# Optimization experiments

Hardware: AMD Instinct MI355X
Metric: run time of the kernel (lower is better)

The kernel has to match this reference:

```python
import jax, jax.numpy as jnp
import numpy as np
import math

B, T, D = 2, 2048, 1024
DC, DM, H = 512, 1536, 16
DE, DG = 4096, 1024
EPS = 1e-5
NEG = -1e30


def _layernorm(x, w, b):
    mu = jnp.mean(x, axis=-1, keepdims=True)
    var = jnp.mean(jnp.square(x - mu), axis=-1, keepdims=True)
    return (x - mu) * jax.lax.rsqrt(var + EPS) * w + b


def setup_inputs() -> dict:
    key = jax.random.key(0)
    ks = jax.random.split(key, 12)
    s = 0.02
    x = jax.random.normal(ks[0], (B, T, D), jnp.float32)
    mask = jnp.tril(jnp.ones((T, T), jnp.int32))[None, None]  # [1,1,T,T] causal
    return {
        "x": x,
        "mask": mask,
        "ln1_w": jnp.ones((D,), jnp.float32),
        "ln1_b": jnp.zeros((D,), jnp.float32),
        "wq": jax.random.normal(ks[1], (D, DC), jnp.float32) * s,
        "bq": jnp.zeros((DC,), jnp.float32),
        "wk": jax.random.normal(ks[2], (D, DC), jnp.float32) * s,
        "bk": jnp.zeros((DC,), jnp.float32),
        "wv": jax.random.normal(ks[3], (D, DM), jnp.float32) * s,
        "bv": jnp.zeros((DM,), jnp.float32),
        "wo": jax.random.normal(ks[4], (DM, D), jnp.float32) * s,
        "bo": jnp.zeros((D,), jnp.float32),
        "ln2_w": jnp.ones((D,), jnp.float32),
        "ln2_b": jnp.zeros((D,), jnp.float32),
        "we": jax.random.normal(ks[5], (D, DE), jnp.float32) * s,
        "be": jnp.zeros((DE,), jnp.float32),
        "wg": jax.random.normal(ks[6], (D, DG), jnp.float32) * s,
        "bg": jnp.zeros((DG,), jnp.float32),
        "wu": jax.random.normal(ks[7], (DG, DE), jnp.float32) * s,
        "bu": jnp.zeros((DE,), jnp.float32),
        "wc": jax.random.normal(ks[8], (DE, D), jnp.float32) * s,
        "bc": jnp.zeros((D,), jnp.float32),
    }


def reference(x, mask, ln1_w, ln1_b, wq, bq, wk, bk, wv, bv, wo, bo,
              ln2_w, ln2_b, we, be, wg, bg, wu, bu, wc, bc):
    b, t, _ = x.shape
    chd, mhd = DC // H, DM // H
    # --- attention sublayer ---
    x1 = _layernorm(x, ln1_w, ln1_b)
    q = (x1 @ wq + bq).reshape(b, t, H, chd).transpose(0, 2, 1, 3)  # [b,h,t,chd]
    k = (x1 @ wk + bk).reshape(b, t, H, chd).transpose(0, 2, 1, 3)
    v = (x1 @ wv + bv).reshape(b, t, H, mhd).transpose(0, 2, 1, 3)  # [b,h,t,mhd]
    sc = jnp.einsum('bhqd,bhkd->bhqk', q, k) / math.sqrt(chd)
    sc = jnp.where(mask == 0, NEG, sc)
    attn = jax.nn.softmax(sc, axis=-1)
    y = jnp.einsum('bhqk,bhkd->bhqd', attn, v)  # [b,h,t,mhd]
    y = y.transpose(0, 2, 1, 3).reshape(b, t, DM)
    x = x + (y @ wo + bo)
    # --- FFN sublayer (double-gated SiLU) ---
    x2 = _layernorm(x, ln2_w, ln2_b)
    e = x2 @ we + be
    g = jax.nn.sigmoid(jax.nn.silu(x2 @ wg + bg) @ wu + bu)
    return x + (jax.nn.silu(e * g) @ wc + bc)
```

## Files before the change

kernel.cpp:

```cpp
#include <hip/hip_runtime.h>
#include <hip/hip_bf16.h>

typedef __bf16 bf16x8_t __attribute__((ext_vector_type(8)));
typedef float f32x4_t __attribute__((ext_vector_type(4)));

#define B_ 2
#define T_ 2048
#define D_ 1024
#define DC_ 512
#define DM_ 1536
#define H_ 16
#define DE_ 4096
#define DG_ 1024
#define ROWS (B_*T_)
#define QS_ 2560
#define EG_ 5120
#define MB (1u<<20)

#define GPTR(p) ((const __attribute__((address_space(1))) unsigned int*)(p))
#define LPTR(p) ((__attribute__((address_space(3))) unsigned int*)(p))

__device__ __forceinline__ float sigmoid_f(float x) { return 1.f / (1.f + __expf(-x)); }

__global__ __launch_bounds__(256)
void transpose_cast(const float* __restrict__ W, __hip_bfloat16* __restrict__ Wt,
                    int K, int N) {
    __shared__ float t[32][33];
    const int n0 = blockIdx.x * 32, k0 = blockIdx.y * 32;
    const int tx = threadIdx.x, ty = threadIdx.y;
#pragma unroll
    for (int r = 0; r < 4; ++r)
        t[ty + r * 8][tx] = W[(size_t)(k0 + ty + r * 8) * N + n0 + tx];
    __syncthreads();
#pragma unroll
    for (int r = 0; r < 4; ++r)
        Wt[(size_t)(n0 + ty + r * 8) * K + k0 + tx] = __float2bfloat16(t[tx][ty + r * 8]);
}

__global__ __launch_bounds__(256)
void concat_bias3(const float* __restrict__ a, int na, const float* __restrict__ b,
                  int nb, const float* __restrict__ c, int n, float* __restrict__ o) {
    const int i = blockIdx.x * 256 + threadIdx.x;
    if (i < n)
        o[i] = i < na ? a[i] : (i < na + nb ? b[i - na] : c[i - na - nb]);
}

__global__ __launch_bounds__(256)
void transpose_v(const __hip_bfloat16* __restrict__ QKV, __hip_bfloat16* __restrict__ Vt) {
    __shared__ __hip_bfloat16 t[32][33];
    const int bh = blockIdx.z;
    const int b = bh >> 4, h = bh & 15;
    const int t0 = blockIdx.x * 32;
    const int d0 = blockIdx.y * 32;
    const int tx = threadIdx.x, ty = threadIdx.y;
#pragma unroll
    for (int r = 0; r < 4; ++r)
        t[ty + r * 8][tx] = QKV[(size_t)(b * T_ + t0 + ty + r * 8) * QS_ + 1024 + h * 96 + d0 + tx];
    __syncthreads();
#pragma unroll
    for (int r = 0; r < 4; ++r)
        Vt[((size_t)bh * 96 + d0 + ty + r * 8) * T_ + t0 + tx] = t[tx][ty + r * 8];
}

__global__ __launch_bounds__(256)
void ln_cast(const float* __restrict__ x, const float* __restrict__ w,
             const float* __restrict__ b, __hip_bfloat16* __restrict__ out) {
    const int row = blockIdx.x;
    const int tid = threadIdx.x;
    const float4 v = ((const float4*)(x + (size_t)row * D_))[tid];
    float s = v.x + v.y + v.z + v.w;
#pragma unroll
    for (int o = 32; o; o >>= 1) s += __shfl_down(s, o);
    __shared__ float red1[4], red2[4];
    if (!(tid & 63)) red1[tid >> 6] = s;
    __syncthreads();
    const float mu = (red1[0] + red1[1] + red1[2] + red1[3]) * (1.f / D_);
    const float dx = v.x - mu, dy = v.y - mu, dz = v.z - mu, dw = v.w - mu;
    float s2 = dx * dx + dy * dy + dz * dz + dw * dw;
#pragma unroll
    for (int o = 32; o; o >>= 1) s2 += __shfl_down(s2, o);
    if (!(tid & 63)) red2[tid >> 6] = s2;
    __syncthreads();
    const float var = (red2[0] + red2[1] + red2[2] + red2[3]) * (1.f / D_);
    const float rs = rsqrtf(var + 1e-5f);
    const float4 wv = ((const float4*)w)[tid];
    const float4 bv = ((const float4*)b)[tid];
    __hip_bfloat16* op = out + (size_t)row * D_ + tid * 4;
    op[0] = __float2bfloat16(dx * rs * wv.x + bv.x);
    op[1] = __float2bfloat16(dy * rs * wv.y + bv.y);
    op[2] = __float2bfloat16(dz * rs * wv.z + bv.z);
    op[3] = __float2bfloat16(dw * rs * wv.w + bv.w);
}

template <int EPI, int BM, int BN>
__global__ __launch_bounds__(256)
void gemm_bt(const __hip_bfloat16* __restrict__ A, const __hip_bfloat16* __restrict__ Bt,
             const float* __restrict__ bias, const float* __restrict__ resid,
             const __hip_bfloat16* __restrict__ Ein,
             void* __restrict__ C0, void* __restrict__ C1, int M, int N, int K) {
    __shared__ __align__(16) __hip_bfloat16 As[BM * 32];
    __shared__ __align__(16) __hip_bfloat16 Bs[BN * 32];
    const int tid = threadIdx.x;
    const int m0 = blockIdx.y * BM;
    const int n0 = blockIdx.x * BN;
    const int lane = tid & 63;
    const int wave = tid >> 6;
    const int wm = (wave >> 1) * (BM / 2), wn = (wave & 1) * (BN / 2);
    const int quad = lane >> 4;
    const int lr = lane & 15;
    constexpr int MI = BM / 32, NJ = BN / 32;

    f32x4_t acc[MI][NJ] = {};

    for (int k0 = 0; k0 < K; k0 += 32) {
#pragma unroll
        for (int p = 0; p < BM / 64; ++p) {
            const int s = p * 256 + tid;
            const int row = s >> 2;
            const int kc2 = (s & 3) ^ ((row >> 1) & 3);
            __builtin_amdgcn_global_load_lds(
                GPTR(A + (size_t)(m0 + row) * K + k0 + kc2 * 8),
                LPTR(&As[s * 8]), 16, 0, 0);
        }
#pragma unroll
        for (int p = 0; p < BN / 64; ++p) {
            const int s = p * 256 + tid;
            const int row = s >> 2;
            const int kc2 = (s & 3) ^ ((row >> 1) & 3);
            __builtin_amdgcn_global_load_lds(
                GPTR(Bt + (size_t)(n0 + row) * K + k0 + kc2 * 8),
                LPTR(&Bs[s * 8]), 16, 0, 0);
        }
        __syncthreads();
        bf16x8_t af[MI], bfr[NJ];
#pragma unroll
        for (int i = 0; i < MI; ++i) {
            const int row = wm + i * 16 + lr;
            af[i] = *(const bf16x8_t*)(&As[(row * 4 + (quad ^ ((row >> 1) & 3))) * 8]);
        }
#pragma unroll
        for (int j = 0; j < NJ; ++j) {
            const int row = wn + j * 16 + lr;
            bfr[j] = *(const bf16x8_t*)(&Bs[(row * 4 + (quad ^ ((row >> 1) & 3))) * 8]);
        }
#pragma unroll
        for (int i = 0; i < MI; ++i)
#pragma unroll
            for (int j = 0; j < NJ; ++j)
                acc[i][j] = __builtin_amdgcn_mfma_f32_16x16x32_bf16(af[i], bfr[j], acc[i][j], 0, 0, 0);
        __syncthreads();
    }

    const int rbase = quad * 4;
#pragma unroll
    for (int j = 0; j < NJ; ++j) {
        const int col = n0 + wn + j * 16 + lr;
        const float bj = bias[col];
#pragma unroll
        for (int i = 0; i < MI; ++i) {
#pragma unroll
            for (int r = 0; r < 4; ++r) {
                const int row = m0 + wm + i * 16 + rbase + r;
                const float v = acc[i][j][r] + bj;
                if (EPI == 0) {
                    ((__hip_bfloat16*)C0)[(size_t)row * N + col] = __float2bfloat16(v);
                } else if (EPI == 1) {
                    const size_t o = (size_t)row * N + col;
                    ((float*)C0)[o] = resid[o] + v;
                } else if (EPI == 4) {
                    const size_t o = (size_t)row * N + col;
                    const float z = __bfloat162float(Ein[o]) * sigmoid_f(v);
                    ((__hip_bfloat16*)C0)[o] = __float2bfloat16(z * sigmoid_f(z));
                } else {
                    if (col < DE_)
                        ((__hip_bfloat16*)C0)[(size_t)row * DE_ + col] = __float2bfloat16(v);
                    else
                        ((__hip_bfloat16*)C1)[(size_t)row * DG_ + (col - DE_)] =
                            __float2bfloat16(v * sigmoid_f(v));
                }
            }
        }
    }
}

__global__ __launch_bounds__(256)
void attn_mfma(const __hip_bfloat16* __restrict__ QKV, const __hip_bfloat16* __restrict__ Vt,
               __hip_bfloat16* __restrict__ Y) {
    __shared__ __hip_bfloat16 Ks[128][40];
    __shared__ __hip_bfloat16 Vts[96][136];
    __shared__ __hip_bfloat16 Ps[4][16][72];
    const int tid = threadIdx.x;
    const int lane = tid & 63;
    const int w = tid >> 6;
    const int c = lane & 15;
    const int quad = lane >> 4;
    const int bh = blockIdx.y;
    const int b = bh >> 4, h = bh & 15;
    const size_t qbase = (size_t)b * T_ * QS_ + h * 32;
    const size_t kbase = qbase + 512;
    const size_t vtbase = (size_t)bh * 96 * T_;
    const size_t ybase = (size_t)b * T_ * DM_ + h * 96;
    const float scale2 = 0.17677669529663687f * 1.4426950408889634f;

    for (int half = 0; half < 2; ++half) {
        const int qt = half ? (31 - (int)blockIdx.x) : (int)blockIdx.x;
        const int q0 = qt * 64;
        const int ntiles = (qt >> 1) + 1;
        const int qrow_a = q0 + w * 16 + c;
        const bf16x8_t qf = *(const bf16x8_t*)(QKV + qbase + (size_t)qrow_a * QS_ + quad * 8);

        f32x4_t o[6] = {};
        float mrow[4], lrow[4];
#pragma unroll
        for (int r = 0; r < 4; ++r) { mrow[r] = -1e30f; lrow[r] = 0.f; }
        const int row_c = q0 + w * 16 + quad * 4;

        for (int t = 0; t < ntiles; ++t) {
            const int k0 = t * 128;
#pragma unroll
            for (int p = 0; p < 2; ++p) {
                const int idx = p * 256 + tid;
                const int kr = idx >> 2, cc = idx & 3;
                *(uint4*)(&Ks[kr][cc * 8]) =
                    *(const uint4*)(QKV + kbase + (size_t)(k0 + kr) * QS_ + cc * 8);
            }
#pragma unroll
            for (int p = 0; p < 6; ++p) {
                const int idx = p * 256 + tid;
                const int vr = idx >> 4, vc = idx & 15;
                *(uint4*)(&Vts[vr][vc * 8]) =
                    *(const uint4*)(Vt + vtbase + (size_t)vr * T_ + k0 + vc * 8);
            }
            __syncthreads();

            f32x4_t s[8];
#pragma unroll
            for (int t2 = 0; t2 < 8; ++t2) {
                const bf16x8_t kf = *(const bf16x8_t*)(&Ks[t2 * 16 + c][quad * 8]);
                f32x4_t z = {0.f, 0.f, 0.f, 0.f};
                s[t2] = __builtin_amdgcn_mfma_f32_16x16x32_bf16(qf, kf, z, 0, 0, 0);
            }

            float p[8][4];
            const bool needmask = (k0 + 128 > q0);
            if (needmask) {
#pragma unroll
                for (int t2 = 0; t2 < 8; ++t2) {
                    const int col = k0 + t2 * 16 + c;
#pragma unroll
                    for (int r = 0; r < 4; ++r) {
                        float v = s[t2][r] * scale2;
                        if (col > row_c + r) v = -1e30f;
                        p[t2][r] = v;
                    }
                }
            } else {
#pragma unroll
                for (int t2 = 0; t2 < 8; ++t2)
#pragma unroll
                    for (int r = 0; r < 4; ++r) p[t2][r] = s[t2][r] * scale2;
            }

#pragma unroll
            for (int r = 0; r < 4; ++r) {
                float mx = p[0][r];
#pragma unroll
                for (int t2 = 1; t2 < 8; ++t2) mx = fmaxf(mx, p[t2][r]);
#pragma unroll
                for (int o2 = 1; o2 < 16; o2 <<= 1) mx = fmaxf(mx, __shfl_xor(mx, o2));
                const float mnew = fmaxf(mrow[r], mx);
                const float alpha = exp2f(mrow[r] - mnew);
                mrow[r] = mnew;
                float rsum = 0.f;
#pragma unroll
                for (int t2 = 0; t2 < 8; ++t2) {
                    p[t2][r] = exp2f(p[t2][r] - mnew);
                    rsum += p[t2][r];
                }
#pragma unroll
                for (int o2 = 1; o2 < 16; o2 <<= 1) rsum += __shfl_xor(rsum, o2);
                lrow[r] = lrow[r] * alpha + rsum;
#pragma unroll
                for (int nb = 0; nb < 6; ++nb) o[nb][r] *= alpha;
            }

#pragma unroll
            for (int hh = 0; hh < 2; ++hh) {
#pragma unroll
                for (int t2 = 0; t2 < 4; ++t2)
#pragma unroll
                    for (int r = 0; r < 4; ++r)
                        Ps[w][quad * 4 + r][t2 * 16 + c] = __float2bfloat16(p[hh * 4 + t2][r]);
                const bf16x8_t pf0 = *(const bf16x8_t*)(&Ps[w][c][quad * 8]);
                const bf16x8_t pf1 = *(const bf16x8_t*)(&Ps[w][c][32 + quad * 8]);
#pragma unroll
                for (int nb = 0; nb < 6; ++nb) {
                    const bf16x8_t vf0 = *(const bf16x8_t*)(&Vts[nb * 16 + c][hh * 64 + quad * 8]);
                    o[nb] = __builtin_amdgcn_mfma_f32_16x16x32_bf16(pf0, vf0, o[nb], 0, 0, 0);
                    const bf16x8_t vf1 = *(const bf16x8_t*)(&Vts[nb * 16 + c][hh * 64 + 32 + quad * 8]);
                    o[nb] = __builtin_amdgcn_mfma_f32_16x16x32_bf16(pf1, vf1, o[nb], 0, 0, 0);
                }
            }
            __syncthreads();
        }

#pragma unroll
        for (int r = 0; r < 4; ++r) {
            const float inv = 1.f / lrow[r];
            const size_t rowoff = ybase + (size_t)(row_c + r) * DM_;
#pragma unroll
            for (int nb = 0; nb < 6; ++nb)
                Y[rowoff + nb * 16 + c] = __float2bfloat16(o[nb][r] * inv);
        }
    }
}

extern "C" void kernel_launch(void* const* d_in, const int* in_sizes, int n_in,
                              void* d_out, int out_size, void* d_ws, size_t ws_size,
                              hipStream_t stream) {
    const float* x     = (const float*)d_in[0];
    const float* ln1_w = (const float*)d_in[2];
    const float* ln1_b = (const float*)d_in[3];
    const float* wq = (const float*)d_in[4];  const float* bq = (const float*)d_in[5];
    const float* wk = (const float*)d_in[6];  const float* bk = (const float*)d_in[7];
    const float* wv = (const float*)d_in[8];  const float* bv = (const float*)d_in[9];
    const float* wo = (const float*)d_in[10]; const float* bo = (const float*)d_in[11];
    const float* ln2_w = (const float*)d_in[12];
    const float* ln2_b = (const float*)d_in[13];
    const float* we = (const float*)d_in[14]; const float* be = (const float*)d_in[15];
    const float* wg = (const float*)d_in[16]; const float* bg = (const float*)d_in[17];
    const float* wu = (const float*)d_in[18]; const float* bu = (const float*)d_in[19];
    const float* wc = (const float*)d_in[20]; const float* bc = (const float*)d_in[21];
    float* out = (float*)d_out;

    char* ws = (char*)d_ws;
    typedef __hip_bfloat16 bf16;
    bf16* wqkvT = (bf16*)(ws + (size_t) 0 * MB);
    bf16* wqT   = wqkvT;
    bf16* wkT   = (bf16*)(ws + (size_t) 1 * MB);
    bf16* wvT   = (bf16*)(ws + (size_t) 2 * MB);
    bf16* woT   = (bf16*)(ws + (size_t) 5 * MB);
    bf16* wewgT = (bf16*)(ws + (size_t) 8 * MB);
    bf16* weT   = wewgT;
    bf16* wgT   = (bf16*)(ws + (size_t)16 * MB);
    bf16* wuT   = (bf16*)(ws + (size_t)18 * MB);
    bf16* wcT   = (bf16*)(ws + (size_t)26 * MB);
    float* bqkv = (float*)(ws + (size_t)34 * MB);
    float* bewg = (float*)(ws + (size_t)34 * MB + 65536);
    bf16* x1b   = (bf16*)(ws + (size_t)35 * MB);
    bf16* x2b   = x1b;
    bf16* qkv   = (bf16*)(ws + (size_t)43 * MB);
    float* xmid = (float*)(ws + (size_t)43 * MB);
    bf16* vt    = (bf16*)(ws + (size_t)63 * MB);
    bf16* yb    = (bf16*)(ws + (size_t)75 * MB);
    bf16* eb    = (bf16*)(ws + (size_t)59 * MB);
    bf16* hb    = (bf16*)(ws + (size_t)91 * MB);

    const dim3 tb(32, 8);
    transpose_cast<<<dim3(DC_ / 32, D_ / 32), tb, 0, stream>>>(wq, wqT, D_, DC_);
    transpose_cast<<<dim3(DC_ / 32, D_ / 32), tb, 0, stream>>>(wk, wkT, D_, DC_);
    transpose_cast<<<dim3(DM_ / 32, D_ / 32), tb, 0, stream>>>(wv, wvT, D_, DM_);
    transpose_cast<<<dim3(D_ / 32, DM_ / 32), tb, 0, stream>>>(wo, woT, DM_, D_);
    transpose_cast<<<dim3(DE_ / 32, D_ / 32), tb, 0, stream>>>(we, weT, D_, DE_);
    transpose_cast<<<dim3(DG_ / 32, D_ / 32), tb, 0, stream>>>(wg, wgT, D_, DG_);
    transpose_cast<<<dim3(DE_ / 32, DG_ / 32), tb, 0, stream>>>(wu, wuT, DG_, DE_);
    transpose_cast<<<dim3(D_ / 32, DE_ / 32), tb, 0, stream>>>(wc, wcT, DE_, D_);
    concat_bias3<<<(QS_ + 255) / 256, 256, 0, stream>>>(bq, 512, bk, 512, bv, QS_, bqkv);
    concat_bias3<<<(EG_ + 255) / 256, 256, 0, stream>>>(be, DE_, bg, DG_, nullptr, EG_, bewg);

    ln_cast<<<ROWS, 256, 0, stream>>>(x, ln1_w, ln1_b, x1b);

    gemm_bt<0, 128, 128><<<dim3(QS_ / 128, ROWS / 128), 256, 0, stream>>>(
        x1b, wqkvT, bqkv, nullptr, nullptr, qkv, nullptr, ROWS, QS_, D_);

    transpose_v<<<dim3(T_ / 32, 3, B_ * H_), tb, 0, stream>>>(qkv, vt);

    attn_mfma<<<dim3(16, B_ * H_), 256, 0, stream>>>(qkv, vt, yb);

    gemm_bt<1, 64, 64><<<dim3(D_ / 64, ROWS / 64), 256, 0, stream>>>(
        yb, woT, bo, x, nullptr, xmid, nullptr, ROWS, D_, DM_);

    ln_cast<<<ROWS, 256, 0, stream>>>(xmid, ln2_w, ln2_b, x2b);

    gemm_bt<5, 128, 128><<<dim3(EG_ / 128, ROWS / 128), 256, 0, stream>>>(
        x2b, wewgT, bewg, nullptr, nullptr, eb, hb, ROWS, EG_, D_);

    gemm_bt<4, 128, 128><<<dim3(DE_ / 128, ROWS / 128), 256, 0, stream>>>(
        hb, wuT, bu, nullptr, eb, eb, nullptr, ROWS, DE_, DG_);

    gemm_bt<1, 64, 64><<<dim3(D_ / 64, ROWS / 64), 256, 0, stream>>>(
        eb, wcT, bc, xmid, nullptr, out, nullptr, ROWS, D_, DE_);
}
```

Measured before the change: 566.5 us.

## Double-buffer GEMM LDS tiles and stage epilogue through LDS for vector stores

The GEMM main loop now uses two LDS buffers, issuing the async global-to-LDS loads for the next K slice before computing the current one, with one barrier per iteration. This hides load latency behind the MFMA work. The epilogue writes accumulators into LDS, then reads them back as 16-byte rows for coalesced vector stores and residual/Ein loads, replacing scattered scalar stores. The cost is more LDS per block, which can reduce occupancy, and the EPI 4 sigmoid result is now rounded to bf16 before the multiply.

```diff
diff --git a/kernel.cpp b/kernel.cpp
--- a/kernel.cpp
+++ b/kernel.cpp
@@ -98,8 +98,17 @@
              const float* __restrict__ bias, const float* __restrict__ resid,
              const __hip_bfloat16* __restrict__ Ein,
              void* __restrict__ C0, void* __restrict__ C1, int M, int N, int K) {
-    __shared__ __align__(16) __hip_bfloat16 As[BM * 32];
-    __shared__ __align__(16) __hip_bfloat16 Bs[BN * 32];
+    constexpr int MI = BM / 32, NJ = BN / 32;
+    constexpr size_t STAGE_BYTES = (size_t)(BM + BN) * 128;
+    constexpr size_t EPI_BYTES = (EPI == 1) ? (size_t)BM * (BN + 4) * 4
+                                            : (size_t)BM * (BN + 8) * 2;
+    constexpr size_t SMEM_BYTES = STAGE_BYTES > EPI_BYTES ? STAGE_BYTES : EPI_BYTES;
+    __shared__ __align__(16) unsigned char smem[SMEM_BYTES];
+    __hip_bfloat16* As0 = (__hip_bfloat16*)smem;
+    __hip_bfloat16* Bs0 = As0 + BM * 32;
+    __hip_bfloat16* As1 = Bs0 + BN * 32;
+    __hip_bfloat16* Bs1 = As1 + BM * 32;
+
     const int tid = threadIdx.x;
     const int m0 = blockIdx.y * BM;
     const int n0 = blockIdx.x * BN;
@@ -108,11 +117,8 @@
     const int wm = (wave >> 1) * (BM / 2), wn = (wave & 1) * (BN / 2);
     const int quad = lane >> 4;
     const int lr = lane & 15;
-    constexpr int MI = BM / 32, NJ = BN / 32;
-
-    f32x4_t acc[MI][NJ] = {};
-
-    for (int k0 = 0; k0 < K; k0 += 32) {
+
+    auto stage = [&](int k0, __hip_bfloat16* Asd, __hip_bfloat16* Bsd) {
 #pragma unroll
         for (int p = 0; p < BM / 64; ++p) {
             const int s = p * 256 + tid;
@@ -120,7 +126,7 @@
             const int kc2 = (s & 3) ^ ((row >> 1) & 3);
             __builtin_amdgcn_global_load_lds(
                 GPTR(A + (size_t)(m0 + row) * K + k0 + kc2 * 8),
-                LPTR(&As[s * 8]), 16, 0, 0);
+                LPTR(Asd + s * 8), 16, 0, 0);
         }
 #pragma unroll
         for (int p = 0; p < BN / 64; ++p) {
@@ -129,55 +135,105 @@
             const int kc2 = (s & 3) ^ ((row >> 1) & 3);
             __builtin_amdgcn_global_load_lds(
                 GPTR(Bt + (size_t)(n0 + row) * K + k0 + kc2 * 8),
-                LPTR(&Bs[s * 8]), 16, 0, 0);
-        }
+                LPTR(Bsd + s * 8), 16, 0, 0);
+        }
+    };
+
+    f32x4_t acc[MI][NJ] = {};
+    stage(0, As0, Bs0);
+    const int kiters = K >> 5;
+    for (int k = 0; k < kiters; ++k) {
         __syncthreads();
+        const __hip_bfloat16* Ar = (k & 1) ? As1 : As0;
+        const __hip_bfloat16* Br = (k & 1) ? Bs1 : Bs0;
+        if (k + 1 < kiters)
+            stage((k + 1) << 5, (k & 1) ? As0 : As1, (k & 1) ? Bs0 : Bs1);
         bf16x8_t af[MI], bfr[NJ];
 #pragma unroll
         for (int i = 0; i < MI; ++i) {
             const int row = wm + i * 16 + lr;
-            af[i] = *(const bf16x8_t*)(&As[(row * 4 + (quad ^ ((row >> 1) & 3))) * 8]);
+            af[i] = *(const bf16x8_t*)(Ar + (row * 4 + (quad ^ ((row >> 1) & 3))) * 8);
         }
 #pragma unroll
         for (int j = 0; j < NJ; ++j) {
             const int row = wn + j * 16 + lr;
-            bfr[j] = *(const bf16x8_t*)(&Bs[(row * 4 + (quad ^ ((row >> 1) & 3))) * 8]);
+            bfr[j] = *(const bf16x8_t*)(Br + (row * 4 + (quad ^ ((row >> 1) & 3))) * 8);
         }
 #pragma unroll
         for (int i = 0; i < MI; ++i)
 #pragma unroll
             for (int j = 0; j < NJ; ++j)
                 acc[i][j] = __builtin_amdgcn_mfma_f32_16x16x32_bf16(af[i], bfr[j], acc[i][j], 0, 0, 0);
+    }
+    __syncthreads();
+
+    if (EPI == 1) {
+        float* Ct = (float*)smem;
+        constexpr int LDC = BN + 4;
+#pragma unroll
+        for (int j = 0; j < NJ; ++j) {
+            const float bj = bias[n0 + wn + j * 16 + lr];
+#pragma unroll
+            for (int i = 0; i < MI; ++i)
+#pragma unroll
+                for (int r = 0; r < 4; ++r)
+                    Ct[(wm + i * 16 + quad * 4 + r) * LDC + wn + j * 16 + lr] =
+                        acc[i][j][r] + bj;
+        }
         __syncthreads();
-    }
-
-    const int rbase = quad * 4;
-#pragma unroll
-    for (int j = 0; j < NJ; ++j) {
-        const int col = n0 + wn + j * 16 + lr;
-        const float bj = bias[col];
-#pragma unroll
-        for (int i = 0; i < MI; ++i) {
-#pragma unroll
-            for (int r = 0; r < 4; ++r) {
-                const int row = m0 + wm + i * 16 + rbase + r;
-                const float v = acc[i][j][r] + bj;
-                if (EPI == 0) {
-                    ((__hip_bfloat16*)C0)[(size_t)row * N + col] = __float2bfloat16(v);
-                } else if (EPI == 1) {
-                    const size_t o = (size_t)row * N + col;
-                    ((float*)C0)[o] = resid[o] + v;
-                } else if (EPI == 4) {
-                    const size_t o = (size_t)row * N + col;
-                    const float z = __bfloat162float(Ein[o]) * sigmoid_f(v);
-                    ((__hip_bfloat16*)C0)[o] = __float2bfloat16(z * sigmoid_f(z));
-                } else {
-                    if (col < DE_)
-                        ((__hip_bfloat16*)C0)[(size_t)row * DE_ + col] = __float2bfloat16(v);
-                    else
-                        ((__hip_bfloat16*)C1)[(size_t)row * DG_ + (col - DE_)] =
-                            __float2bfloat16(v * sigmoid_f(v));
+        constexpr int CH = BN / 4;
+#pragma unroll
+        for (int p = 0; p < BM * CH / 256; ++p) {
+            const int s = p * 256 + tid;
+            const int row = s / CH, ch = s % CH;
+            float4 t = *(const float4*)(&Ct[row * LDC + ch * 4]);
+            const size_t o = (size_t)(m0 + row) * N + n0 + ch * 4;
+            const float4 rv = *(const float4*)(resid + o);
+            t.x += rv.x; t.y += rv.y; t.z += rv.z; t.w += rv.w;
+            *(float4*)((float*)C0 + o) = t;
+        }
+    } else {
+        __hip_bfloat16* Ct = (__hip_bfloat16*)smem;
+        constexpr int LDC = BN + 8;
+        const bool gsilu = (EPI == 5) && (n0 >= DE_);
+#pragma unroll
+        for (int j = 0; j < NJ; ++j) {
+            const float bj = bias[n0 + wn + j * 16 + lr];
+#pragma unroll
+            for (int i = 0; i < MI; ++i)
+#pragma unroll
+                for (int r = 0; r < 4; ++r) {
+                    float v = acc[i][j][r] + bj;
+                    if (EPI == 4) v = sigmoid_f(v);
+                    else if (EPI == 5) { if (gsilu) v = v * sigmoid_f(v); }
+                    Ct[(wm + i * 16 + quad * 4 + r) * LDC + wn + j * 16 + lr] =
+                        __float2bfloat16(v);
                 }
+        }
+        __syncthreads();
+        constexpr int CH = BN / 8;
+#pragma unroll
+        for (int p = 0; p < BM * CH / 256; ++p) {
+            const int s = p * 256 + tid;
+            const int row = s / CH, ch = s % CH;
+            union { uint4 u; __hip_bfloat16 h[8]; } tv, ev, ov;
+            tv.u = *(const uint4*)(&Ct[row * LDC + ch * 8]);
+            if (EPI == 4) {
+                const size_t o = (size_t)(m0 + row) * N + n0 + ch * 8;
+                ev.u = *(const uint4*)(Ein + o);
+#pragma unroll
+                for (int q = 0; q < 8; ++q) {
+                    const float z = __bfloat162float(ev.h[q]) * __bfloat162float(tv.h[q]);
+                    ov.h[q] = __float2bfloat16(z * sigmoid_f(z));
+                }
+                *(uint4*)((__hip_bfloat16*)C0 + o) = ov.u;
+            } else if (EPI == 5) {
+                if (n0 < DE_)
+                    *(uint4*)((__hip_bfloat16*)C0 + (size_t)(m0 + row) * DE_ + n0 + ch * 8) = tv.u;
+                else
+                    *(uint4*)((__hip_bfloat16*)C1 + (size_t)(m0 + row) * DG_ + (n0 - DE_) + ch * 8) = tv.u;
+            } else {
+                *(uint4*)((__hip_bfloat16*)C0 + (size_t)(m0 + row) * N + n0 + ch * 8) = tv.u;
             }
         }
     }
```

Result: faster. 517.6 us (-8.6%).
